# Kernel optimization log

Hardware: AMD Instinct MI355X
Metric: run time of the kernel (lower is better)

Reference implementation:

```python
import jax, jax.numpy as jnp
import numpy as np

H = 64   # gru_hidden_dim == gnn_hidden_dim
F = 64   # node_feat_dim
K = 8    # k_nn
OUT = 32 # output_factor_dim
BN_EPS = 1e-5


def _gru_scan(x, Wih, Whh, bih, bhh):
    # x: [S, F] single sequence (torch bug makes GRU scan the b*n axis); returns [S, H]
    xp = x @ Wih.T + bih  # [S, 3H], gate order r,z,n (torch convention)
    def step(h, xt):
        hp = h @ Whh.T + bhh
        r = jax.nn.sigmoid(xt[:H] + hp[:H])
        z = jax.nn.sigmoid(xt[H:2 * H] + hp[H:2 * H])
        ng = jnp.tanh(xt[2 * H:] + r * hp[2 * H:])
        hn = (1.0 - z) * ng + z * h
        return hn, hn
    _, out = jax.lax.scan(step, jnp.zeros((H,), x.dtype), xp)
    return out


def _gcn_layer(x, row, col, w, W, b, n):
    # PyG GCNConv: out[col] += d^{-1/2}[row] * w * d^{-1/2}[col] * (x @ W.T)[row] + b
    xw = x @ W.T
    deg = jnp.zeros((n,), x.dtype).at[col].add(w)
    dinv = deg ** -0.5
    dinv = jnp.where(jnp.isinf(dinv), 0.0, dinv)
    norm = dinv[row] * w * dinv[col]
    out = jnp.zeros_like(xw).at[col].add(norm[:, None] * xw[row])
    return out + b


def setup_inputs() -> dict:
    key = jax.random.key(0)
    ks = jax.random.split(key, 20)
    s = 0.08  # ~ torch uniform(-1/sqrt(64), 1/sqrt(64)) scale
    d = {
        'x_seq': jax.random.normal(ks[0], (4, 8, F, 2048), jnp.float32),
        # gru_sim params
        'Wih_s': jax.random.normal(ks[1], (3 * H, F), jnp.float32) * s,
        'Whh_s': jax.random.normal(ks[2], (3 * H, H), jnp.float32) * s,
        'bih_s': jax.random.normal(ks[3], (3 * H,), jnp.float32) * s,
        'bhh_s': jax.random.normal(ks[4], (3 * H,), jnp.float32) * s,
        # gru params
        'Wih': jax.random.normal(ks[5], (3 * H, F), jnp.float32) * s,
        'Whh': jax.random.normal(ks[6], (3 * H, H), jnp.float32) * s,
        'bih': jax.random.normal(ks[7], (3 * H,), jnp.float32) * s,
        'bhh': jax.random.normal(ks[8], (3 * H,), jnp.float32) * s,
        # gcn1 / gcn2 params (GCNConv weight [out,in], bias [out])
        'W1': jax.random.normal(ks[9], (H, H), jnp.float32) * s,
        'b1': jnp.zeros((H,), jnp.float32),
        'W2': jax.random.normal(ks[10], (H, H), jnp.float32) * s,
        'b2': jnp.zeros((H,), jnp.float32),
        # batchnorm affine
        'gamma': jnp.ones((H,), jnp.float32),
        'beta': jnp.zeros((H,), jnp.float32),
        # predictor
        'Wp': jax.random.normal(ks[11], (OUT, H), jnp.float32) * s,
        'bp': jnp.zeros((OUT,), jnp.float32),
    }
    return d


def reference(x_seq, Wih_s, Whh_s, bih_s, bhh_s, Wih, Whh, bih, bhh,
              W1, b1, W2, b2, gamma, beta, Wp, bp):
    b, l, f, n = x_seq.shape
    # torch GRU is batch_first=True but fed [l, b*n, f]: it scans the b*n axis
    # as time and gru_out[-1] keeps only batch item l-1 -> only last time slice used.
    seq = x_seq[:, -1].transpose(0, 2, 1).reshape(b * n, f)  # [b*n, f]
    h = _gru_scan(seq, Wih_s, Whh_s, bih_s, bhh_s).reshape(b, n, H)      # gru_sim
    h_out = _gru_scan(seq, Wih, Whh, bih, bhh).reshape(b, n, H)          # gru

    # dynamic kNN graph from similarity
    sim = jnp.einsum('bni,bmi->bnm', h, h)
    eye = jnp.eye(n, dtype=bool)
    sim = jnp.where(eye[None], jnp.asarray(-1e9, sim.dtype), sim)
    vals, idx = jax.lax.top_k(sim, K)  # [b, n, K], sorted desc like torch.topk

    # edges: n*K knn edges + n unit-weight self loops (outer add_self_loops;
    # GCNConv's add_remaining_self_loops then adds nothing)
    row = jnp.concatenate([jnp.repeat(jnp.arange(n), K), jnp.arange(n)])

    def per_graph(v, ix, x):
        col = jnp.concatenate([ix.reshape(-1), jnp.arange(n)])
        w = jnp.concatenate([v.reshape(-1), jnp.ones((n,), v.dtype)])
        o1 = jax.nn.relu(_gcn_layer(x, row, col, w, W1, b1, n))
        o2 = jax.nn.relu(_gcn_layer(o1, row, col, w, W2, b2, n))
        return o2

    out2 = jax.vmap(per_graph)(vals, idx, h_out)  # [b, n, H]

    # BatchNorm1d (training mode: biased batch stats over b*n rows)
    flat = out2.reshape(b * n, H)
    mu = flat.mean(0)
    var = flat.var(0)
    normed = (flat - mu) / jnp.sqrt(var + BN_EPS) * gamma + beta

    out = normed @ Wp.T + bp
    return out.reshape(b, n, OUT)
```

## Files before the change

### kernel.cpp

```cpp
#include <hip/hip_runtime.h>
#include <hip/hip_bf16.h>

typedef __hip_bfloat16 bf16;

#define NB   4
#define NN   2048
#define NROW 8192
#define HD   64
#define G3   192
#define KNN  8
#define OUTD 32
#define SCHUNK 32
#define SBURN  96
#define NCH    256
#define SCH4   32
#define SBRN4  64
#define NCH4   256
#define TI   4
#define TOPB 256
#define XPR  32
#define SCR  32
#define TKR  16

#define OFF_FLAG  0u
#define OFF_DEG   64u
#define OFF_DINV  8256u
#define OFF_BNS   16448u
#define OFF_BNSQ  16512u
#define OFF_SCALE 16576u
#define OFF_SHIFT 16640u
#define OFF_VALS  16704u
#define OFF_IDX   82240u
#define OFF_A     147776u
#define OFF_C     672064u
#define OFF_XP0   1196352u
#define OFF_XP1   2769216u
#define OFF_END   4342080u

typedef __attribute__((ext_vector_type(8))) short short8v;
typedef __attribute__((ext_vector_type(4))) float f32x4;

__device__ __forceinline__ float sigmoidf_(float x) { return 1.f / (1.f + __expf(-x)); }
__device__ __forceinline__ float tanhf_(float x) {
    float e = __expf(-2.f * fabsf(x));
    float t = (1.f - e) / (1.f + e);
    return copysignf(t, x);
}
__device__ __forceinline__ float ld(const void* p, size_t i, int isbf) {
    return isbf ? __bfloat162float(((const bf16*)p)[i]) : ((const float*)p)[i];
}
__device__ __forceinline__ float bcast(float v, int k) {
    return __int_as_float(__builtin_amdgcn_readlane(__float_as_int(v), k));
}
__device__ __forceinline__ unsigned short bf16rne(float f) {
    unsigned u = __float_as_uint(f);
    return (unsigned short)((u + 0x7FFFu + ((u >> 16) & 1u)) >> 16);
}

__global__ void probe_kernel(const void* __restrict__ gamma, int* __restrict__ flag)
{
    unsigned w = ((const unsigned*)gamma)[0];
    *flag = (w == 0x3F800000u) ? 0 : 1;
}

__global__ __launch_bounds__(384) void xp_kernel(
    const void* __restrict__ x_seq,
    const void* __restrict__ Wih_s, const void* __restrict__ bih_s,
    const void* __restrict__ Wih,   const void* __restrict__ bih,
    float* __restrict__ xp0, float* __restrict__ xp1,
    const int* __restrict__ dtp)
{
    int isbf = *dtp;
    int row0 = blockIdx.x * XPR;
    int b = row0 >> 11, j0 = row0 & 2047;
    int t = threadIdx.x;

    __shared__ __align__(16) float S[XPR * 68];
    for (int idx = t; idx < XPR * HD; idx += 384) {
        int f = idx >> 5, jj = idx & (XPR - 1);
        S[jj * 68 + f] = ld(x_seq, (size_t)((b * 8 + 7) * 64 + f) * 2048 + (j0 + jj), isbf);
    }

    int g = t % G3;
    const void* W  = (t < G3) ? Wih_s : Wih;
    const void* bi = (t < G3) ? bih_s : bih;
    float* o = (t < G3) ? xp0 : xp1;
    float wreg[64];
    #pragma unroll
    for (int k = 0; k < 64; ++k) wreg[k] = ld(W, g * HD + k, isbf);
    float bias = ld(bi, g, isbf);
    __syncthreads();

    for (int jj = 0; jj < XPR; ++jj) {
        const float4* s4 = (const float4*)(S + jj * 68);
        float a0 = bias, a1 = 0.f, a2 = 0.f, a3 = 0.f;
        #pragma unroll
        for (int q = 0; q < 16; ++q) {
            float4 v = s4[q];
            a0 += wreg[4*q+0] * v.x;
            a1 += wreg[4*q+1] * v.y;
            a2 += wreg[4*q+2] * v.z;
            a3 += wreg[4*q+3] * v.w;
        }
        o[(size_t)(row0 + jj) * G3 + g] = (a0 + a1) + (a2 + a3);
    }
}

__global__ __launch_bounds__(64) void gru_scan_pack_kernel(
    const float* __restrict__ xp0, const float* __restrict__ xp1,
    const void* __restrict__ Whh_s, const void* __restrict__ bhh_s,
    const void* __restrict__ Whh,   const void* __restrict__ bhh,
    unsigned short* __restrict__ hAhi, unsigned short* __restrict__ hAlo,
    float* __restrict__ hC,
    const int* __restrict__ dtp)
{
    int isbf = *dtp;
    int gru   = blockIdx.x >> 8;
    int chunk = blockIdx.x & (NCH4 - 1);
    const float* xpp = gru ? xp1 : xp0;
    const void* Wh   = gru ? Whh : Whh_s;
    const void* bh_p = gru ? bhh : bhh_s;

    int L = threadIdx.x;

    __shared__ __align__(16) float4 SW4[64 * 64];

    for (int k = 0; k < 64; ++k) {
        float4 v;
        v.x = ld(Wh, (size_t)L * 64 + k, isbf);
        v.y = ld(Wh, (size_t)(64 + L) * 64 + k, isbf);
        v.z = ld(Wh, (size_t)(128 + L) * 64 + k, isbf);
        v.w = 0.f;
        SW4[k * 64 + L] = v;
    }
    float br  = ld(bh_p, L, isbf);
    float bz  = ld(bh_p, 64 + L, isbf);
    float bn_ = ld(bh_p, 128 + L, isbf);
    __syncthreads();

    int first = chunk * SCH4;
    int burn  = min(SBRN4, first);
    int start = first - burn;
    int steps = burn + SCH4;

    float hval = 0.f;
    size_t rb = (size_t)start * G3;
    float xr = xpp[rb + L];
    float xz = xpp[rb + 64 + L];
    float xn = xpp[rb + 128 + L];

    for (int t = 0; t < steps; ++t) {
        size_t nb = (size_t)min(start + t + 1, NROW - 1) * G3;
        float pxr = xpp[nb + L];
        float pxz = xpp[nb + 64 + L];
        float pxn = xpp[nb + 128 + L];

        float pr0 = br, pz0 = bz, pn0 = bn_;
        float pr1 = 0.f, pz1 = 0.f, pn1 = 0.f;
        #pragma unroll
        for (int k = 0; k < 64; k += 2) {
            float4 w0 = SW4[k * 64 + L];
            float4 w1 = SW4[(k + 1) * 64 + L];
            float b0 = bcast(hval, k);
            float b1 = bcast(hval, k + 1);
            pr0 += w0.x * b0; pz0 += w0.y * b0; pn0 += w0.z * b0;
            pr1 += w1.x * b1; pz1 += w1.y * b1; pn1 += w1.z * b1;
        }

        float r  = sigmoidf_(xr + pr0 + pr1);
        float z  = sigmoidf_(xz + pz0 + pz1);
        float ng = tanhf_(xn + r * (pn0 + pn1));
        hval = (1.f - z) * ng + z * hval;

        if (t >= burn) {
            size_t o = (size_t)(start + t) * HD + L;
            if (gru) {
                hC[o] = hval;
            } else {
                unsigned short hb = bf16rne(hval);
                float hf = __uint_as_float(((unsigned)hb) << 16);
                hAhi[o] = hb;
                hAlo[o] = bf16rne(hval - hf);
            }
        }
        xr = pxr; xz = pxz; xn = pxn;
    }
}

__global__ __launch_bounds__(192, 2) void gru_scan_fused_kernel(
    const void* __restrict__ x_seq,
    const void* __restrict__ Wih_s, const void* __restrict__ bih_s,
    const void* __restrict__ Whh_s, const void* __restrict__ bhh_s,
    const void* __restrict__ Wih,   const void* __restrict__ bih,
    const void* __restrict__ Whh,   const void* __restrict__ bhh,
    float* __restrict__ hA, float* __restrict__ hC,
    const int* __restrict__ dtp)
{
    int isbf = *dtp;
    int gru   = blockIdx.x >> 8;
    int chunk = blockIdx.x & 255;
    const void* Wh = gru ? Whh : Whh_s;
    const void* bh_p = gru ? bhh : bhh_s;
    const void* Wi = gru ? Wih : Wih_s;
    const void* bi_p = gru ? bih : bih_s;
    float* hout = gru ? hC : hA;

    int lane = threadIdx.x & 63;
    int w    = threadIdx.x >> 6;
    int g    = w * 64 + lane;

    float whh[64], wih[64];
    #pragma unroll
    for (int k = 0; k < 64; ++k) {
        whh[k] = ld(Wh, g * 64 + k, isbf);
        wih[k] = ld(Wi, g * 64 + k, isbf);
    }
    float bh = ld(bh_p, g, isbf);
    float bi = ld(bi_p, g, isbf);

    __shared__ float hs[64];
    __shared__ float ss[64];
    __shared__ float gr[64], gz[64], ga[64], gx[64];

    int first = chunk * SCHUNK;
    int burn  = min(SBURN, first);
    int start = first - burn;
    int steps = burn + SCHUNK;

    #define XIDX(r) ((size_t)((((r) >> 11) * 8 + 7) * 64 + lane) * 2048 + ((r) & 2047))
    float sf = 0.f;
    if (w == 0) {
        ss[lane] = ld(x_seq, XIDX(start), isbf);
        if (steps > 1) sf = ld(x_seq, XIDX(start + 1), isbf);
    }
    __syncthreads();

    float hval = 0.f;
    float sval = ss[lane];

    for (int t = 0; t < steps; ++t) {
        float a = bh, x = bi;
        #pragma unroll
        for (int k = 0; k < 64; ++k) {
            a += whh[k] * bcast(hval, k);
            x += wih[k] * bcast(sval, k);
        }
        if (w == 0)      gr[lane] = sigmoidf_(x + a);
        else if (w == 1) gz[lane] = sigmoidf_(x + a);
        else           { ga[lane] = a; gx[lane] = x; }
        __syncthreads();
        if (w == 0) {
            if (t + 1 < steps) {
                ss[lane] = sf;
                if (t + 2 < steps) sf = ld(x_seq, XIDX(start + t + 2), isbf);
            }
        } else if (w == 2) {
            float hn = (1.f - gz[lane]) * tanhf_(gx[lane] + gr[lane] * ga[lane])
                     + gz[lane] * hval;
            hs[lane] = hn;
            hval = hn;
            if (t >= burn) hout[(size_t)(start + t) * HD + lane] = hn;
        }
        __syncthreads();
        if (w != 2) hval = hs[lane];
        sval = ss[lane];
    }
    #undef XIDX
}

__device__ __forceinline__ void merge8(float tv[KNN], int tj[KNN], int off)
{
    float ov[KNN]; int oj[KNN];
    #pragma unroll
    for (int m = 0; m < KNN; ++m) {
        ov[m] = __shfl_xor(tv[m], off);
        oj[m] = __shfl_xor(tj[m], off);
    }
    #pragma unroll
    for (int m = 0; m < KNN; ++m) {
        if (ov[KNN - 1 - m] > tv[m]) { tv[m] = ov[KNN - 1 - m]; tj[m] = oj[KNN - 1 - m]; }
    }
    #pragma unroll
    for (int d = 4; d > 0; d >>= 1) {
        #pragma unroll
        for (int m = 0; m < KNN; ++m) {
            if ((m & d) == 0 && (m | d) < KNN) {
                int p = m | d;
                if (tv[p] > tv[m]) {
                    float fv = tv[m]; tv[m] = tv[p]; tv[p] = fv;
                    int fj = tj[m]; tj[m] = tj[p]; tj[p] = fj;
                }
            }
        }
    }
}

__global__ __launch_bounds__(256) void topk_mfma_kernel(
    const unsigned short* __restrict__ Ahi, const unsigned short* __restrict__ Alo,
    float* __restrict__ vals, int* __restrict__ idxs, float* __restrict__ deg)
{
    int bid = blockIdx.x;
    int row0 = bid * TKR;
    int bbase = row0 & ~(NN - 1);
    int rloc = row0 & (NN - 1);
    int t = threadIdx.x;
    int w = t >> 6, L = t & 63;
    int cL = L & 15, q = L >> 4;
    int chunk = q * 8;

    __shared__ __align__(16) float sw[4][64 * 20];
    __shared__ float mv[4][TKR][KNN];
    __shared__ int   mj[4][TKR][KNN];

    size_t arow = (size_t)(row0 + cL) * HD;
    short8v ahi0 = *(const short8v*)(Ahi + arow + chunk);
    short8v ahi1 = *(const short8v*)(Ahi + arow + 32 + chunk);
    short8v alo0 = *(const short8v*)(Alo + arow + chunk);
    short8v alo1 = *(const short8v*)(Alo + arow + 32 + chunk);

    int jbase = w * 512;
    float* swv = sw[w];
    int r = L >> 2, p = L & 3;

    float tv[KNN]; int tj[KNN];
    #pragma unroll
    for (int m = 0; m < KNN; ++m) { tv[m] = -3e38f; tj[m] = 0; }

    #pragma unroll 1
    for (int strip = 0; strip < 8; ++strip) {
        #pragma unroll
        for (int g = 0; g < 4; ++g) {
            int j0 = jbase + strip * 64 + g * 16;
            size_t brow = (size_t)(bbase + j0 + cL) * HD;
            short8v bhi0 = *(const short8v*)(Ahi + brow + chunk);
            short8v bhi1 = *(const short8v*)(Ahi + brow + 32 + chunk);
            short8v blo0 = *(const short8v*)(Alo + brow + chunk);
            short8v blo1 = *(const short8v*)(Alo + brow + 32 + chunk);
            f32x4 accA = {0.f, 0.f, 0.f, 0.f};
            f32x4 accB = {0.f, 0.f, 0.f, 0.f};
            accA = __builtin_amdgcn_mfma_f32_16x16x32_bf16(ahi0, bhi0, accA, 0, 0, 0);
            accB = __builtin_amdgcn_mfma_f32_16x16x32_bf16(ahi0, blo0, accB, 0, 0, 0);
            accA = __builtin_amdgcn_mfma_f32_16x16x32_bf16(ahi1, bhi1, accA, 0, 0, 0);
            accB = __builtin_amdgcn_mfma_f32_16x16x32_bf16(ahi1, blo1, accB, 0, 0, 0);
            accA = __builtin_amdgcn_mfma_f32_16x16x32_bf16(alo0, bhi0, accA, 0, 0, 0);
            accB = __builtin_amdgcn_mfma_f32_16x16x32_bf16(alo1, bhi1, accB, 0, 0, 0);
            f32x4 acc = accA + accB;
            *(f32x4*)(swv + (g * 16 + cL) * 20 + q * 4) = acc;
        }
        int cb = jbase + strip * 64;
        #pragma unroll 1
        for (int ci = 0; ci < 16; ++ci) {
            int c = (ci << 2) + p;
            float nv = swv[c * 20 + r];
            int j = cb + c;
            nv = (j == rloc + r) ? -1e9f : nv;
            if (nv > tv[KNN - 1]) {
                tv[KNN - 1] = nv; tj[KNN - 1] = j;
                #pragma unroll
                for (int m = KNN - 1; m > 0; --m) {
                    if (tv[m] > tv[m - 1]) {
                        float fv = tv[m]; tv[m] = tv[m - 1]; tv[m - 1] = fv;
                        int fj = tj[m]; tj[m] = tj[m - 1]; tj[m - 1] = fj;
                    }
                }
            }
        }
    }

    merge8(tv, tj, 1);
    merge8(tv, tj, 2);
    if (p == 0) {
        #pragma unroll
        for (int m = 0; m < KNN; ++m) { mv[w][r][m] = tv[m]; mj[w][r][m] = tj[m]; }
    }
    __syncthreads();

    if (w == 0) {
        int wv = p;
        #pragma unroll
        for (int m = 0; m < KNN; ++m) { tv[m] = mv[wv][r][m]; tj[m] = mj[wv][r][m]; }
        merge8(tv, tj, 1);
        merge8(tv, tj, 2);
        if (wv == 0) {
            int row = row0 + r;
            #pragma unroll
            for (int m = 0; m < KNN; ++m) {
                vals[(size_t)row * KNN + m] = tv[m];
                idxs[(size_t)row * KNN + m] = tj[m];
                atomicAdd(deg + bbase + tj[m], tv[m]);
            }
            atomicAdd(deg + row, 1.0f);
        }
    }
}

__global__ __launch_bounds__(TOPB, 2) void topk_kernel(
    const float* __restrict__ h,
    float* __restrict__ vals, int* __restrict__ idxs, float* __restrict__ deg)
{
    int bid = blockIdx.x;
    int b    = bid >> 9;
    int row0 = b * NN + (bid & 511) * TI;
    int i0 = row0 & 2047;
    int t = threadIdx.x;

    __shared__ __align__(16) float sim[TI][NN];
    __shared__ __align__(16) float hi[TI * HD];

    for (int q = t; q < TI * HD; q += TOPB)
        hi[q] = h[(size_t)(row0 + (q >> 6)) * HD + (q & 63)];
    __syncthreads();

    const float* hb = h + (size_t)b * NN * HD;
    const float4* hi4 = (const float4*)hi;
    #pragma unroll 1
    for (int j = t; j < NN; j += TOPB) {
        const float4* hr = (const float4*)(hb + (size_t)j * HD);
        float acc[TI];
        #pragma unroll
        for (int m = 0; m < TI; ++m) acc[m] = 0.f;
        #pragma unroll 4
        for (int q = 0; q < 16; ++q) {
            float4 v = hr[q];
            #pragma unroll
            for (int m = 0; m < TI; ++m) {
                float4 c = hi4[m * 16 + q];
                acc[m] += v.x*c.x + v.y*c.y + v.z*c.z + v.w*c.w;
            }
        }
        #pragma unroll
        for (int m = 0; m < TI; ++m)
            sim[m][j] = (j == i0 + m) ? -1e9f : acc[m];
    }
    __syncthreads();

    int w    = t >> 6;
    int lane = t & 63;
    int row  = row0 + w;

    float tv[KNN]; int tj[KNN];
    #pragma unroll
    for (int m = 0; m < KNN; ++m) { tv[m] = -3e38f; tj[m] = 0; }

    for (int k = 0; k < 32; ++k) {
        int j = lane + (k << 6);
        float nv = sim[w][j];
        if (nv > tv[KNN - 1]) {
            tv[KNN - 1] = nv; tj[KNN - 1] = j;
            #pragma unroll
            for (int m = KNN - 1; m > 0; --m) {
                if (tv[m] > tv[m - 1]) {
                    float fv = tv[m]; tv[m] = tv[m - 1]; tv[m - 1] = fv;
                    int fj = tj[m]; tj[m] = tj[m - 1]; tj[m - 1] = fj;
                }
            }
        }
    }

    #pragma unroll
    for (int off = 1; off < 64; off <<= 1) {
        float ov[KNN]; int oj[KNN];
        #pragma unroll
        for (int m = 0; m < KNN; ++m) {
            ov[m] = __shfl_xor(tv[m], off);
            oj[m] = __shfl_xor(tj[m], off);
        }
        #pragma unroll
        for (int m = 0; m < KNN; ++m) {
            if (ov[KNN - 1 - m] > tv[m]) { tv[m] = ov[KNN - 1 - m]; tj[m] = oj[KNN - 1 - m]; }
        }
        if (off < 32) {
            #pragma unroll
            for (int d = 4; d > 0; d >>= 1) {
                #pragma unroll
                for (int m = 0; m < KNN; ++m) {
                    if ((m & d) == 0 && (m | d) < KNN) {
                        int p = m | d;
                        if (tv[p] > tv[m]) {
                            float fv = tv[m]; tv[m] = tv[p]; tv[p] = fv;
                            int fj = tj[m]; tj[m] = tj[p]; tj[p] = fj;
                        }
                    }
                }
            }
        }
    }

    if (lane == 0) {
        #pragma unroll
        for (int m = 0; m < KNN; ++m) {
            vals[(size_t)row * KNN + m] = tv[m];
            idxs[(size_t)row * KNN + m] = tj[m];
            atomicAdd(deg + (b << 11) + tj[m], tv[m]);
        }
        atomicAdd(deg + row, 1.0f);
    }
}

__global__ void dinv_kernel(const float* __restrict__ deg, float* __restrict__ dinv)
{
    int g = blockIdx.x * 256 + threadIdx.x;
    if (g >= NROW) return;
    float d = deg[g];
    float r = 1.f / sqrtf(d);
    dinv[g] = isinf(r) ? 0.f : r;
}

__global__ __launch_bounds__(256) void scatter_kernel(
    const float* __restrict__ in, const void* __restrict__ W,
    const void* __restrict__ bias, int dorelu,
    const float* __restrict__ dinv,
    const float* __restrict__ vals, const int* __restrict__ idxs,
    float* __restrict__ acc, const int* __restrict__ dtp)
{
    int isbf = *dtp;
    int lane = threadIdx.x & 63;
    int w    = threadIdx.x >> 6;

    float wreg[64];
    #pragma unroll
    for (int k = 0; k < 64; ++k) wreg[k] = ld(W, lane * HD + k, isbf);
    float bb = ld(bias, lane, isbf);

    int row0 = blockIdx.x * SCR + w * (SCR / 4);
    #pragma unroll 1
    for (int rr = 0; rr < SCR / 4; ++rr) {
        int row = row0 + rr;
        int b = row >> 11;
        float x = in[(size_t)row * HD + lane];
        if (dorelu) x = fmaxf(x + bb, 0.f);
        float v0 = 0.f, v1 = 0.f, v2 = 0.f, v3 = 0.f;
        #pragma unroll
        for (int k = 0; k < 64; k += 4) {
            v0 += wreg[k]     * bcast(x, k);
            v1 += wreg[k + 1] * bcast(x, k + 1);
            v2 += wreg[k + 2] * bcast(x, k + 2);
            v3 += wreg[k + 3] * bcast(x, k + 3);
        }
        float v = (v0 + v1) + (v2 + v3);
        float di = dinv[row];
        atomicAdd(acc + (size_t)row * HD + lane, di * di * v);
        #pragma unroll
        for (int k = 0; k < KNN; ++k) {
            int c = idxs[(size_t)row * KNN + k];
            float wv = vals[(size_t)row * KNN + k];
            float nw = di * wv * dinv[(b << 11) + c];
            atomicAdd(acc + (size_t)((b << 11) + c) * HD + lane, nw * v);
        }
    }
}

__global__ void bn_stats_kernel(const float* __restrict__ acc2, const void* __restrict__ bias,
                                float* __restrict__ bns, float* __restrict__ bnsq,
                                const int* __restrict__ dtp)
{
    int isbf = *dtp;
    int c = blockIdx.x;
    int t = threadIdx.x;
    float bb = ld(bias, c, isbf);
    float s = 0.f, s2 = 0.f;
    for (int r = t; r < NROW; r += 256) {
        float v = fmaxf(acc2[(size_t)r * HD + c] + bb, 0.f);
        s += v; s2 += v * v;
    }
    __shared__ float sv[4], sv2[4];
    #pragma unroll
    for (int off = 32; off > 0; off >>= 1) {
        s  += __shfl_down(s, off);
        s2 += __shfl_down(s2, off);
    }
    if ((t & 63) == 0) { sv[t >> 6] = s; sv2[t >> 6] = s2; }
    __syncthreads();
    if (t == 0) {
        for (int w = 1; w < 4; ++w) { s += sv[w]; s2 += sv2[w]; }
        bns[c] = s; bnsq[c] = s2;
    }
}

__global__ void bn_final_kernel(const float* __restrict__ bns, const float* __restrict__ bnsq,
                                const void* __restrict__ gamma, const void* __restrict__ beta,
                                float* __restrict__ scale, float* __restrict__ shift,
                                const int* __restrict__ dtp)
{
    int isbf = *dtp;
    int c = threadIdx.x;
    float mu = bns[c] / (float)NROW;
    float var = fmaxf(bnsq[c] / (float)NROW - mu * mu, 0.f);
    float sc = ld(gamma, c, isbf) / sqrtf(var + 1e-5f);
    scale[c] = sc;
    shift[c] = ld(beta, c, isbf) - mu * sc;
}

__global__ void out_kernel(const float* __restrict__ acc2, const void* __restrict__ bias2,
                           const float* __restrict__ scale, const float* __restrict__ shift,
                           const void* __restrict__ Wp, const void* __restrict__ bp,
                           float* __restrict__ out, const int* __restrict__ dtp)
{
    int isbf = *dtp;
    int row0 = blockIdx.x * 2;
    int t = threadIdx.x;
    __shared__ float nl[2 * HD];
    for (int q = t; q < 2 * HD; q += 64) {
        int r = q >> 6, c = q & (HD - 1);
        float v = fmaxf(acc2[(size_t)(row0 + r) * HD + c] + ld(bias2, c, isbf), 0.f);
        nl[q] = v * scale[c] + shift[c];
    }
    __syncthreads();
    int rr = t >> 5, o = t & 31;
    float acc = ld(bp, o, isbf);
    #pragma unroll
    for (int k = 0; k < HD; ++k) acc += nl[rr * HD + k] * ld(Wp, o * HD + k, isbf);
    out[(size_t)(row0 + rr) * OUTD + o] = acc;
}

extern "C" void kernel_launch(void* const* d_in, const int* in_sizes, int n_in,
                              void* d_out, int out_size, void* d_ws, size_t ws_size,
                              hipStream_t stream)
{
    (void)in_sizes; (void)n_in; (void)out_size;
    const void* x_seq = d_in[0];
    const void* Wih_s = d_in[1];
    const void* Whh_s = d_in[2];
    const void* bih_s = d_in[3];
    const void* bhh_s = d_in[4];
    const void* Wih   = d_in[5];
    const void* Whh   = d_in[6];
    const void* bih   = d_in[7];
    const void* bhh   = d_in[8];
    const void* W1    = d_in[9];
    const void* b1    = d_in[10];
    const void* W2    = d_in[11];
    const void* b2    = d_in[12];
    const void* gamma = d_in[13];
    const void* beta  = d_in[14];
    const void* Wp    = d_in[15];
    const void* bp    = d_in[16];
    float* out = (float*)d_out;

    float* ws = (float*)d_ws;
    int*   dtp  = (int*)(ws + OFF_FLAG);
    float* deg  = ws + OFF_DEG;
    float* dinv = ws + OFF_DINV;
    float* bns  = ws + OFF_BNS;
    float* bnsq = ws + OFF_BNSQ;
    float* scale = ws + OFF_SCALE;
    float* shift = ws + OFF_SHIFT;
    float* vals = ws + OFF_VALS;
    int*   idxs = (int*)(ws + OFF_IDX);
    float* A    = ws + OFF_A;
    float* C    = ws + OFF_C;
    float* xp0  = ws + OFF_XP0;
    float* xp1  = ws + OFF_XP1;

    bool big_ws = ws_size >= (size_t)OFF_END * sizeof(float);

    probe_kernel<<<1, 1, 0, stream>>>(gamma, dtp);
    hipMemsetAsync(deg, 0, NROW * sizeof(float), stream);

    if (big_ws) {
        xp_kernel<<<NROW / XPR, 384, 0, stream>>>(x_seq, Wih_s, bih_s, Wih, bih, xp0, xp1, dtp);
        gru_scan_pack_kernel<<<2 * NCH4, 64, 0, stream>>>(
            xp0, xp1, Whh_s, bhh_s, Whh, bhh,
            (unsigned short*)A, (unsigned short*)A + (size_t)NROW * HD, C, dtp);
        topk_mfma_kernel<<<NROW / TKR, 256, 0, stream>>>(
            (unsigned short*)A, (unsigned short*)A + (size_t)NROW * HD, vals, idxs, deg);
    } else {
        gru_scan_fused_kernel<<<2 * NCH, 192, 0, stream>>>(x_seq, Wih_s, bih_s, Whh_s, bhh_s,
                                                           Wih, bih, Whh, bhh, A, C, dtp);
        topk_kernel<<<NROW / TI, TOPB, 0, stream>>>(A, vals, idxs, deg);
    }
    dinv_kernel<<<NROW / 256, 256, 0, stream>>>(deg, dinv);

    hipMemsetAsync(A, 0, (size_t)NROW * HD * sizeof(float), stream);
    scatter_kernel<<<NROW / SCR, 256, 0, stream>>>(C, W1, b1, 0, dinv, vals, idxs, A, dtp);

    hipMemsetAsync(C, 0, (size_t)NROW * HD * sizeof(float), stream);
    scatter_kernel<<<NROW / SCR, 256, 0, stream>>>(A, W2, b1, 1, dinv, vals, idxs, C, dtp);

    bn_stats_kernel<<<HD, 256, 0, stream>>>(C, b2, bns, bnsq, dtp);
    bn_final_kernel<<<1, HD, 0, stream>>>(bns, bnsq, gamma, beta, scale, shift, dtp);
    out_kernel<<<NROW / 2, 64, 0, stream>>>(C, b2, scale, shift, Wp, bp, out, dtp);
}
```

Before: 396.6 us.

## Interleave two GRU scan chunks per wavefront to hide recurrence latency

Each 64-thread block now advances two independent sequence chunks together, sharing the same LDS weight reads, with the shorter chunk delayed so both finish on the same step. The dependent matvec and gate chains of the two chunks interleave, which is meant to give the serial recurrence more instruction-level parallelism and halve the number of blocks and weight-staging passes. The cost is more registers per thread and fewer blocks in flight on the GPU.

```diff
diff --git a/kernel.cpp b/kernel.cpp
--- a/kernel.cpp
+++ b/kernel.cpp
@@ -13,9 +13,7 @@
 #define SCHUNK 32
 #define SBURN  96
 #define NCH    256
-#define SCH4   32
-#define SBRN4  64
-#define NCH4   256
+#define NCH5   128
 #define TI   4
 #define TOPB 256
 #define XPR  32
@@ -106,7 +104,7 @@
     }
 }
 
-__global__ __launch_bounds__(64) void gru_scan_pack_kernel(
+__global__ __launch_bounds__(64) void gru_scan_pair_kernel(
     const float* __restrict__ xp0, const float* __restrict__ xp1,
     const void* __restrict__ Whh_s, const void* __restrict__ bhh_s,
     const void* __restrict__ Whh,   const void* __restrict__ bhh,
@@ -115,8 +113,8 @@
     const int* __restrict__ dtp)
 {
     int isbf = *dtp;
-    int gru   = blockIdx.x >> 8;
-    int chunk = blockIdx.x & (NCH4 - 1);
+    int gru = blockIdx.x >> 7;
+    int pb  = blockIdx.x & (NCH5 - 1);
     const float* xpp = gru ? xp1 : xp0;
     const void* Wh   = gru ? Whh : Whh_s;
     const void* bh_p = gru ? bhh : bhh_s;
@@ -138,52 +136,88 @@
     float bn_ = ld(bh_p, 128 + L, isbf);
     __syncthreads();
 
-    int first = chunk * SCH4;
-    int burn  = min(SBRN4, first);
-    int start = first - burn;
-    int steps = burn + SCH4;
-
-    float hval = 0.f;
-    size_t rb = (size_t)start * G3;
-    float xr = xpp[rb + L];
-    float xz = xpp[rb + 64 + L];
-    float xn = xpp[rb + 128 + L];
-
-    for (int t = 0; t < steps; ++t) {
-        size_t nb = (size_t)min(start + t + 1, NROW - 1) * G3;
-        float pxr = xpp[nb + L];
-        float pxz = xpp[nb + 64 + L];
-        float pxn = xpp[nb + 128 + L];
-
-        float pr0 = br, pz0 = bz, pn0 = bn_;
-        float pr1 = 0.f, pz1 = 0.f, pn1 = 0.f;
+    int first0 = pb * 64;
+    int first1 = first0 + 32;
+    int burn0  = min(64, first0);
+    int burn1  = min(64, first1);
+    int start0 = first0 - burn0;
+    int start1 = first1 - burn1;
+    int steps0 = burn0 + 32;
+    int steps1 = burn1 + 32;
+    int tmax   = steps1;
+    int d0     = tmax - steps0;
+
+    float hA_ = 0.f, hB_ = 0.f;
+    float xrA = xpp[(size_t)start0 * G3 + L];
+    float xzA = xpp[(size_t)start0 * G3 + 64 + L];
+    float xnA = xpp[(size_t)start0 * G3 + 128 + L];
+    float xrB = xpp[(size_t)start1 * G3 + L];
+    float xzB = xpp[(size_t)start1 * G3 + 64 + L];
+    float xnB = xpp[(size_t)start1 * G3 + 128 + L];
+
+    for (int t = 0; t < tmax; ++t) {
+        int nA = start0 + min(max(t + 1 - d0, 0), steps0 - 1);
+        int nB = start1 + min(t + 1, tmax - 1);
+        float pxrA = xpp[(size_t)nA * G3 + L];
+        float pxzA = xpp[(size_t)nA * G3 + 64 + L];
+        float pxnA = xpp[(size_t)nA * G3 + 128 + L];
+        float pxrB = xpp[(size_t)nB * G3 + L];
+        float pxzB = xpp[(size_t)nB * G3 + 64 + L];
+        float pxnB = xpp[(size_t)nB * G3 + 128 + L];
+
+        float prA0 = br, pzA0 = bz, pnA0 = bn_;
+        float prA1 = 0.f, pzA1 = 0.f, pnA1 = 0.f;
+        float prB0 = br, pzB0 = bz, pnB0 = bn_;
+        float prB1 = 0.f, pzB1 = 0.f, pnB1 = 0.f;
         #pragma unroll
         for (int k = 0; k < 64; k += 2) {
             float4 w0 = SW4[k * 64 + L];
             float4 w1 = SW4[(k + 1) * 64 + L];
-            float b0 = bcast(hval, k);
-            float b1 = bcast(hval, k + 1);
-            pr0 += w0.x * b0; pz0 += w0.y * b0; pn0 += w0.z * b0;
-            pr1 += w1.x * b1; pz1 += w1.y * b1; pn1 += w1.z * b1;
-        }
-
-        float r  = sigmoidf_(xr + pr0 + pr1);
-        float z  = sigmoidf_(xz + pz0 + pz1);
-        float ng = tanhf_(xn + r * (pn0 + pn1));
-        hval = (1.f - z) * ng + z * hval;
-
-        if (t >= burn) {
-            size_t o = (size_t)(start + t) * HD + L;
+            float a0 = bcast(hA_, k);
+            float a1 = bcast(hA_, k + 1);
+            float b0 = bcast(hB_, k);
+            float b1 = bcast(hB_, k + 1);
+            prA0 += w0.x * a0; pzA0 += w0.y * a0; pnA0 += w0.z * a0;
+            prA1 += w1.x * a1; pzA1 += w1.y * a1; pnA1 += w1.z * a1;
+            prB0 += w0.x * b0; pzB0 += w0.y * b0; pnB0 += w0.z * b0;
+            prB1 += w1.x * b1; pzB1 += w1.y * b1; pnB1 += w1.z * b1;
+        }
+
+        float rA  = sigmoidf_(xrA + prA0 + prA1);
+        float zA  = sigmoidf_(xzA + pzA0 + pzA1);
+        float ngA = tanhf_(xnA + rA * (pnA0 + pnA1));
+        float hnA = (1.f - zA) * ngA + zA * hA_;
+        hA_ = (t >= d0) ? hnA : 0.f;
+
+        float rB  = sigmoidf_(xrB + prB0 + prB1);
+        float zB  = sigmoidf_(xzB + pzB0 + pzB1);
+        float ngB = tanhf_(xnB + rB * (pnB0 + pnB1));
+        hB_ = (1.f - zB) * ngB + zB * hB_;
+
+        if (t >= d0 + burn0) {
+            size_t o = (size_t)(start0 + t - d0) * HD + L;
             if (gru) {
-                hC[o] = hval;
+                hC[o] = hA_;
             } else {
-                unsigned short hb = bf16rne(hval);
+                unsigned short hb = bf16rne(hA_);
                 float hf = __uint_as_float(((unsigned)hb) << 16);
                 hAhi[o] = hb;
-                hAlo[o] = bf16rne(hval - hf);
-            }
-        }
-        xr = pxr; xz = pxz; xn = pxn;
+                hAlo[o] = bf16rne(hA_ - hf);
+            }
+        }
+        if (t >= burn1) {
+            size_t o = (size_t)(start1 + t) * HD + L;
+            if (gru) {
+                hC[o] = hB_;
+            } else {
+                unsigned short hb = bf16rne(hB_);
+                float hf = __uint_as_float(((unsigned)hb) << 16);
+                hAhi[o] = hb;
+                hAlo[o] = bf16rne(hB_ - hf);
+            }
+        }
+        xrA = pxrA; xzA = pxzA; xnA = pxnA;
+        xrB = pxrB; xzB = pxzB; xnB = pxnB;
     }
 }
 
@@ -659,7 +693,7 @@
 
     if (big_ws) {
         xp_kernel<<<NROW / XPR, 384, 0, stream>>>(x_seq, Wih_s, bih_s, Wih, bih, xp0, xp1, dtp);
-        gru_scan_pack_kernel<<<2 * NCH4, 64, 0, stream>>>(
+        gru_scan_pair_kernel<<<2 * NCH5, 64, 0, stream>>>(
             xp0, xp1, Whh_s, bhh_s, Whh, bhh,
             (unsigned short*)A, (unsigned short*)A + (size_t)NROW * HD, C, dtp);
         topk_mfma_kernel<<<NROW / TKR, 256, 0, stream>>>(
```

New measurement: 425.7 us. +7.3%, slower.
